# Kernel tuning notes

Measured on AMD Instinct MI355X. Metric: run time of the kernel, lower is better.

The kernel has to match this reference:

```python
import jax, jax.numpy as jnp
import numpy as np

N = 50000      # nodes
E = 1_600_000  # edges
F_IN = 128; HID = 128; LAT = 64; OUT = 128; GEN = 2


def gcn_conv(x, src, dst, norm, W, b, n_nodes):
    """PyG GCNConv with self-loops already appended to (src, dst) and
    symmetric normalization `norm` precomputed per edge."""
    h = x @ W                                    # [N, out]
    msg = h[src] * norm[:, None]                 # [E+N, out] gather + scale
    out = jax.ops.segment_sum(msg, dst, num_segments=n_nodes)
    return out + b


def _self_loop_norm(edge_index, n_nodes):
    loops = jnp.arange(n_nodes, dtype=edge_index.dtype)
    src = jnp.concatenate([edge_index[0], loops])
    dst = jnp.concatenate([edge_index[1], loops])
    deg = jnp.zeros((n_nodes,), jnp.float32).at[dst].add(1.0)
    dinv = jnp.where(deg > 0, deg ** -0.5, 0.0)
    norm = dinv[src] * dinv[dst]
    return src, dst, norm


def setup_inputs() -> dict:
    key = jax.random.key(0)
    ks = jax.random.split(key, 12)
    p = lambda k, s: jax.random.normal(k, s, jnp.float32) * 0.05
    return {
        "x": jax.random.normal(ks[0], (N, F_IN), jnp.float32),
        "edge_index": jax.random.randint(ks[1], (2, E), 0, N, jnp.int32),
        "eps": jax.random.normal(ks[2], (N, LAT), jnp.float32),
        "u": jax.random.uniform(ks[3], (N, GEN), jnp.float32),
        "W1": p(ks[4], (F_IN, HID)), "b1": jnp.zeros((HID,), jnp.float32),
        "W_mu": p(ks[5], (HID, LAT)), "b_mu": jnp.zeros((LAT,), jnp.float32),
        "W_ls": p(ks[6], (HID, LAT)), "b_ls": jnp.zeros((LAT,), jnp.float32),
        "W_dx": p(ks[7], (LAT, OUT)), "b_dx": jnp.zeros((OUT,), jnp.float32),
        "W_g": p(ks[8], (LAT, GEN)), "b_g": jnp.zeros((GEN,), jnp.float32),
        "W_lc": p(ks[9], (LAT, 1)), "b_lc": jnp.zeros((1,), jnp.float32),
    }


def reference(x, edge_index, eps, u, W1, b1, W_mu, b_mu, W_ls, b_ls,
              W_dx, b_dx, W_g, b_g, W_lc, b_lc):
    n = x.shape[0]
    src, dst, norm = _self_loop_norm(edge_index, n)

    # Encoder: GCN -> relu -> (mu, logvar)
    h = jax.nn.relu(gcn_conv(x, src, dst, norm, W1, b1, n))
    mu = gcn_conv(h, src, dst, norm, W_mu, b_mu, n)
    logvar = gcn_conv(h, src, dst, norm, W_ls, b_ls, n)

    # reparameterize: z = eps * exp(0.5*logvar) + mu
    z = eps * jnp.exp(0.5 * logvar) + mu

    # decoders / classifiers
    recon_x = gcn_conv(z, src, dst, norm, W_dx, b_dx, n)
    logits_gender = gcn_conv(z, src, dst, norm, W_g, b_g, n)
    logits_label = z @ W_lc + b_lc

    # Gumbel-softmax (hard, straight-through), temperature=1.0
    g = -jnp.log(-jnp.log(u + 1e-20) + 1e-20)
    y_soft = jax.nn.softmax(logits_gender + g, axis=-1)
    y_hard = jax.nn.one_hot(jnp.argmax(y_soft, axis=-1), GEN, dtype=y_soft.dtype)
    gender = jax.lax.stop_gradient(y_hard - y_soft) + y_soft

    return (recon_x, gender, logits_label, mu, logvar, z)
```

## Files before the change

kernel.cpp:

```cpp
#include <hip/hip_runtime.h>
#include <hip/hip_fp16.h>
#include <cstddef>


constexpr int R = 200;
constexpr int NBUCK = 250;
constexpr int NBLK = 250;
constexpr int SLABCAP = 12288;

__device__ __forceinline__ void gemm_tile32(
    int tile, const float* __restrict__ A, const float* __restrict__ W,
    __half* __restrict__ Ch, int n, float* sW) {
  constexpr int K = 128, M = 128, KT = 64, RPT = 4, CG = 32;
  const int tid = threadIdx.x;
  const int cgi = tid % CG;
  const int rs = tid / CG;
  const int row0 = tile * 32 + rs * RPT;

  const float* Arow[RPT];
#pragma unroll
  for (int rr = 0; rr < RPT; ++rr) {
    int row = row0 + rr;
    if (row > n - 1) row = n - 1;
    Arow[rr] = A + (size_t)row * K;
  }
  float4 acc[RPT];
#pragma unroll
  for (int rr = 0; rr < RPT; ++rr) acc[rr] = float4{0.f, 0.f, 0.f, 0.f};

  for (int kt = 0; kt < K; kt += KT) {
    if (kt) __syncthreads();
    for (int i = tid * 4; i < KT * M; i += 1024)
      *reinterpret_cast<float4*>(&sW[i]) =
          *reinterpret_cast<const float4*>(&W[kt * M + i]);
    __syncthreads();
#pragma unroll 4
    for (int k4 = 0; k4 < KT; k4 += 4) {
      float4 a[RPT];
#pragma unroll
      for (int rr = 0; rr < RPT; ++rr)
        a[rr] = *reinterpret_cast<const float4*>(Arow[rr] + kt + k4);
#pragma unroll
      for (int j = 0; j < 4; ++j) {
        float4 w2 = *reinterpret_cast<const float4*>(&sW[(k4 + j) * M + cgi * 4]);
#pragma unroll
        for (int rr = 0; rr < RPT; ++rr) {
          float av = reinterpret_cast<const float*>(&a[rr])[j];
          acc[rr].x += av * w2.x; acc[rr].y += av * w2.y;
          acc[rr].z += av * w2.z; acc[rr].w += av * w2.w;
        }
      }
    }
  }
#pragma unroll
  for (int rr = 0; rr < RPT; ++rr) {
    int row = row0 + rr;
    if (row < n) {
      __half2* d2 = reinterpret_cast<__half2*>(Ch + (size_t)row * M + cgi * 4);
      d2[0] = __floats2half2_rn(acc[rr].x, acc[rr].y);
      d2[1] = __floats2half2_rn(acc[rr].z, acc[rr].w);
    }
  }
}

union HistSmem { int h[NBUCK]; float sW[64 * 128]; };
__global__ __launch_bounds__(256, 4) void hist_gemm_kernel(
    const int* __restrict__ dst, int* __restrict__ gh, int e, int chunk,
    const float* __restrict__ A, const float* __restrict__ W,
    __half* __restrict__ Ch, int n, int tbase) {
  __shared__ HistSmem sm;
  if (blockIdx.x < (unsigned)NBLK) {
    for (int t = threadIdx.x; t < NBUCK; t += 256) sm.h[t] = 0;
    __syncthreads();
    int beg = blockIdx.x * chunk;
    int fin = min(e, beg + chunk);
    for (int i = beg + threadIdx.x; i < fin; i += 256)
      atomicAdd(&sm.h[dst[i] / R], 1);
    __syncthreads();
    for (int t = threadIdx.x; t < NBUCK; t += 256)
      gh[t * NBLK + blockIdx.x] = sm.h[t];
  } else {
    gemm_tile32(tbase + (blockIdx.x - NBLK), A, W, Ch, n, sm.sW);
  }
}

union BscanSmem { struct { int s[256]; int sBase[NBUCK + 1]; } b; float sW[64 * 128]; };
__global__ __launch_bounds__(256, 4) void bscan_gemm_kernel(
    const int* __restrict__ gh, int* __restrict__ ghs,
    int* __restrict__ rowptr_n,
    const float* __restrict__ A, const float* __restrict__ W,
    __half* __restrict__ Ch, int n, int tbase) {
  __shared__ BscanSmem sm;
  const int tid = threadIdx.x;
  if (blockIdx.x < (unsigned)NBUCK) {
    const int b = blockIdx.x;
    int tot = 0;
    if (tid < NBUCK) {
      const int* row = gh + tid * NBLK;
      for (int k = 0; k < NBLK; ++k) tot += row[k];
    }
    sm.b.s[tid] = tot;
    __syncthreads();
    for (int off = 1; off < 256; off <<= 1) {
      int t = (tid >= off) ? sm.b.s[tid - off] : 0;
      __syncthreads();
      sm.b.s[tid] += t;
      __syncthreads();
    }
    if (tid < NBUCK) sm.b.sBase[tid] = sm.b.s[tid] - tot;
    if (tid == NBUCK - 1) sm.b.sBase[NBUCK] = sm.b.s[tid];
    __syncthreads();

    int v = (tid < NBLK) ? gh[b * NBLK + tid] : 0;
    sm.b.s[tid] = v;
    __syncthreads();
    for (int off = 1; off < 256; off <<= 1) {
      int t = (tid >= off) ? sm.b.s[tid - off] : 0;
      __syncthreads();
      sm.b.s[tid] += t;
      __syncthreads();
    }
    if (tid < NBLK) ghs[b * NBLK + tid] = sm.b.s[tid] - v + sm.b.sBase[b];
    if (b == 0 && tid == 0) *rowptr_n = sm.b.sBase[NBUCK];
  } else {
    gemm_tile32(tbase + (blockIdx.x - NBUCK), A, W, Ch, n, sm.sW);
  }
}

union ScatSmem { int cur[NBUCK]; float sW[64 * 128]; };
__global__ __launch_bounds__(256, 4) void scatter_gemm_kernel(
    const int* __restrict__ src, const int* __restrict__ dst,
    const int* __restrict__ ghs, int* __restrict__ binned, int e, int chunk,
    const float* __restrict__ A, const float* __restrict__ W,
    __half* __restrict__ Ch, int n, int tbase) {
  __shared__ ScatSmem sm;
  if (blockIdx.x < (unsigned)NBLK) {
    for (int t = threadIdx.x; t < NBUCK; t += 256)
      sm.cur[t] = ghs[t * NBLK + blockIdx.x];
    __syncthreads();
    int beg = blockIdx.x * chunk;
    int fin = min(e, beg + chunk);
    for (int i = beg + threadIdx.x; i < fin; i += 256) {
      int d = dst[i];
      int b = d / R;
      int p = atomicAdd(&sm.cur[b], 1);
      binned[p] = ((d - b * R) << 16) | src[i];
    }
  } else {
    gemm_tile32(tbase + (blockIdx.x - NBLK), A, W, Ch, n, sm.sW);
  }
}

union FinSmem {
  struct { int sdeg[R]; int sscan[256]; int scur[R]; int slab[SLABCAP]; } f;
  float sW[64 * 128];
};
__global__ __launch_bounds__(256, 3) void final_gemm_kernel(
    const int* __restrict__ binned, const int* __restrict__ ghs,
    int* __restrict__ rowptr, int* __restrict__ csr,
    float* __restrict__ dinv, int n, int e,
    const float* __restrict__ A, const float* __restrict__ W,
    __half* __restrict__ Ch, int tbase, int T) {
  __shared__ FinSmem sm;
  const int tid = threadIdx.x;
  if (blockIdx.x < (unsigned)NBUCK) {
    const int b = blockIdx.x;
    const int base = ghs[b * NBLK];
    const int endv = (b < NBUCK - 1) ? ghs[(b + 1) * NBLK] : e;
    const int cnt = endv - base;

    if (tid < R) sm.f.sdeg[tid] = 0;
    __syncthreads();
    for (int k = base + tid; k < endv; k += 256)
      atomicAdd(&sm.f.sdeg[binned[k] >> 16], 1);
    __syncthreads();

    int dv = (tid < R) ? sm.f.sdeg[tid] : 0;
    sm.f.sscan[tid] = dv;
    __syncthreads();
    for (int off = 1; off < 256; off <<= 1) {
      int t = (tid >= off) ? sm.f.sscan[tid - off] : 0;
      __syncthreads();
      sm.f.sscan[tid] += t;
      __syncthreads();
    }
    int excl = sm.f.sscan[tid] - dv;
    int node = b * R + tid;
    if (tid < R && node < n) {
      rowptr[node] = base + excl;
      dinv[node] = 1.0f / sqrtf((float)dv + 1.0f);
      sm.f.scur[tid] = excl;
    }
    __syncthreads();

    const bool fits = (cnt <= SLABCAP);
    for (int k = base + tid; k < endv; k += 256) {
      int rec = binned[k];
      int p = atomicAdd(&sm.f.scur[rec >> 16], 1);
      int s = rec & 0xFFFF;
      if (fits) sm.f.slab[p] = s;
      else csr[base + p] = s;
    }
    __syncthreads();
    if (fits)
      for (int k = tid; k < cnt; k += 256) csr[base + k] = sm.f.slab[k];
  } else {
    int t0 = tbase + (blockIdx.x - NBUCK);
    if (t0 < T) gemm_tile32(t0, A, W, Ch, n, sm.sW);
  }
}

template <int K, int M, int KT, int RPT, bool BIAS>
__global__ __launch_bounds__(256, 4) void gemm_kernel(
    const float* __restrict__ A, const float* __restrict__ W,
    const float* __restrict__ bias, float* __restrict__ C, int n) {
  constexpr int CG = M / 4;
  constexpr int RS = 256 / CG;
  constexpr int RPB = RS * RPT;
  __shared__ float sW[KT * M];
  const int cg = threadIdx.x % CG;
  const int rs = threadIdx.x / CG;
  const int row0 = blockIdx.x * RPB + rs * RPT;

  const float* Arow[RPT];
#pragma unroll
  for (int rr = 0; rr < RPT; ++rr) {
    int row = row0 + rr;
    if (row > n - 1) row = n - 1;
    Arow[rr] = A + (size_t)row * K;
  }

  float4 acc[RPT];
#pragma unroll
  for (int rr = 0; rr < RPT; ++rr) acc[rr] = float4{0.f, 0.f, 0.f, 0.f};

  for (int kt = 0; kt < K; kt += KT) {
    if (kt) __syncthreads();
    for (int i = threadIdx.x * 4; i < KT * M; i += 1024)
      *reinterpret_cast<float4*>(&sW[i]) =
          *reinterpret_cast<const float4*>(&W[kt * M + i]);
    __syncthreads();
#pragma unroll 4
    for (int k4 = 0; k4 < KT; k4 += 4) {
      float4 a[RPT];
#pragma unroll
      for (int rr = 0; rr < RPT; ++rr)
        a[rr] = *reinterpret_cast<const float4*>(Arow[rr] + kt + k4);
#pragma unroll
      for (int j = 0; j < 4; ++j) {
        float4 w = *reinterpret_cast<const float4*>(&sW[(k4 + j) * M + cg * 4]);
#pragma unroll
        for (int rr = 0; rr < RPT; ++rr) {
          float av = reinterpret_cast<const float*>(&a[rr])[j];
          acc[rr].x += av * w.x;
          acc[rr].y += av * w.y;
          acc[rr].z += av * w.z;
          acc[rr].w += av * w.w;
        }
      }
    }
  }

  float4 bv = float4{0.f, 0.f, 0.f, 0.f};
  if (BIAS) bv = *reinterpret_cast<const float4*>(&bias[cg * 4]);
#pragma unroll
  for (int rr = 0; rr < RPT; ++rr) {
    int row = row0 + rr;
    if (row < n) {
      float4 o = acc[rr];
      if (BIAS) { o.x += bv.x; o.y += bv.y; o.z += bv.z; o.w += bv.w; }
      *reinterpret_cast<float4*>(&C[(size_t)row * M + cg * 4]) = o;
    }
  }
}

template <bool SRCSCALE, bool BIAS, bool RELU, bool HALF_OUT>
__global__ __launch_bounds__(256) void spmm128_kernel(
    const __half* __restrict__ Xs, void* __restrict__ Yout,
    const int* __restrict__ rowptr, const int* __restrict__ csr,
    const float* __restrict__ dinv, const float* __restrict__ bias, int n) {
  int wid = (blockIdx.x * blockDim.x + threadIdx.x) >> 6;
  int lane = threadIdx.x & 63;
  if (wid >= n) return;
  int beg = rowptr[wid];
  int end = rowptr[wid + 1];
  constexpr int U = 8;
  float a0[U], a1[U];
#pragma unroll
  for (int uu = 0; uu < U; ++uu) { a0[uu] = 0.f; a1[uu] = 0.f; }

  for (int base = beg; base < end; base += 64) {
    int m = end - base;
    if (m > 64) m = 64;
    int idx = (lane < m) ? csr[base + lane] : 0;
    int j = 0;
    for (; j + U <= m; j += U) {
      const __half2* rows[U];
      float ds[U];
#pragma unroll
      for (int uu = 0; uu < U; ++uu) {
        int i = __shfl(idx, j + uu, 64);
        rows[uu] = reinterpret_cast<const __half2*>(Xs + (size_t)i * 128);
        if (SRCSCALE) ds[uu] = dinv[i];
      }
      __half2 v[U];
#pragma unroll
      for (int uu = 0; uu < U; ++uu) v[uu] = rows[uu][lane];
#pragma unroll
      for (int uu = 0; uu < U; ++uu) {
        float2 f = __half22float2(v[uu]);
        if (SRCSCALE) {
          a0[uu] += ds[uu] * f.x;
          a1[uu] += ds[uu] * f.y;
        } else {
          a0[uu] += f.x;
          a1[uu] += f.y;
        }
      }
    }
    for (; j < m; ++j) {
      int i = __shfl(idx, j, 64);
      const __half2* row = reinterpret_cast<const __half2*>(Xs + (size_t)i * 128);
      float2 f = __half22float2(row[lane]);
      if (SRCSCALE) {
        float ds = dinv[i];
        a0[0] += ds * f.x;
        a1[0] += ds * f.y;
      } else {
        a0[0] += f.x;
        a1[0] += f.y;
      }
    }
  }

  float t0 = 0.f, t1 = 0.f;
#pragma unroll
  for (int uu = 0; uu < U; ++uu) { t0 += a0[uu]; t1 += a1[uu]; }

  float di = dinv[wid];

  float2 sf = __half22float2(
      reinterpret_cast<const __half2*>(Xs + (size_t)wid * 128)[lane]);
  if (SRCSCALE) {
    t0 += di * sf.x;
    t1 += di * sf.y;
  } else {
    t0 += sf.x;
    t1 += sf.y;
  }

  float r0 = di * t0;
  float r1 = di * t1;
  if (BIAS) { r0 += bias[lane * 2]; r1 += bias[lane * 2 + 1]; }
  if (RELU) { r0 = fmaxf(r0, 0.f); r1 = fmaxf(r1, 0.f); }

  if (HALF_OUT) {
    reinterpret_cast<__half2*>((__half*)Yout + (size_t)wid * 128)[lane] =
        __floats2half2_rn(di * r0, di * r1);
  } else {
    float2 o = {r0, r1};
    reinterpret_cast<float2*>((float*)Yout + (size_t)wid * 128)[lane] = o;
  }
}

__global__ __launch_bounds__(256, 4) void mlz_kernel(
    const float* __restrict__ hagg,
    const float* __restrict__ Wmu, const float* __restrict__ bmu,
    const float* __restrict__ Wls, const float* __restrict__ bls,
    const float* __restrict__ eps, const float* __restrict__ dinv,
    const float* __restrict__ Wg, const float* __restrict__ Wlc,
    const float* __restrict__ blc,
    float* __restrict__ out_mu, float* __restrict__ out_lv,
    float* __restrict__ out_z, unsigned int* __restrict__ zh8,
    float2* __restrict__ zgs, float* __restrict__ out_label, int n) {
  constexpr int K = 128, M = 64, KT = 64, RPT = 4;
  constexpr int CG = M / 4;
  constexpr int RS = 256 / CG;
  constexpr int RPB = RS * RPT;
  __shared__ float sWm[KT * M];
  __shared__ float sWl[KT * M];
  const int cg = threadIdx.x % CG;
  const int rs = threadIdx.x / CG;
  const int row0 = blockIdx.x * RPB + rs * RPT;

  const float* Arow[RPT];
#pragma unroll
  for (int rr = 0; rr < RPT; ++rr) {
    int row = row0 + rr;
    if (row > n - 1) row = n - 1;
    Arow[rr] = hagg + (size_t)row * K;
  }

  float4 am[RPT], al[RPT];
#pragma unroll
  for (int rr = 0; rr < RPT; ++rr) {
    am[rr] = float4{0.f, 0.f, 0.f, 0.f};
    al[rr] = float4{0.f, 0.f, 0.f, 0.f};
  }

  for (int kt = 0; kt < K; kt += KT) {
    if (kt) __syncthreads();
    for (int i = threadIdx.x * 4; i < KT * M; i += 1024) {
      *reinterpret_cast<float4*>(&sWm[i]) =
          *reinterpret_cast<const float4*>(&Wmu[kt * M + i]);
      *reinterpret_cast<float4*>(&sWl[i]) =
          *reinterpret_cast<const float4*>(&Wls[kt * M + i]);
    }
    __syncthreads();
#pragma unroll 2
    for (int k4 = 0; k4 < KT; k4 += 4) {
      float4 a[RPT];
#pragma unroll
      for (int rr = 0; rr < RPT; ++rr)
        a[rr] = *reinterpret_cast<const float4*>(Arow[rr] + kt + k4);
#pragma unroll
      for (int j = 0; j < 4; ++j) {
        float4 wm = *reinterpret_cast<const float4*>(&sWm[(k4 + j) * M + cg * 4]);
        float4 wl = *reinterpret_cast<const float4*>(&sWl[(k4 + j) * M + cg * 4]);
#pragma unroll
        for (int rr = 0; rr < RPT; ++rr) {
          float av = reinterpret_cast<const float*>(&a[rr])[j];
          am[rr].x += av * wm.x; am[rr].y += av * wm.y;
          am[rr].z += av * wm.z; am[rr].w += av * wm.w;
          al[rr].x += av * wl.x; al[rr].y += av * wl.y;
          al[rr].z += av * wl.z; al[rr].w += av * wl.w;
        }
      }
    }
  }

  float4 bm = *reinterpret_cast<const float4*>(&bmu[cg * 4]);
  float4 bl = *reinterpret_cast<const float4*>(&bls[cg * 4]);
  float wg0[4], wg1[4], wlcv[4];
#pragma unroll
  for (int cc = 0; cc < 4; ++cc) {
    int c = cg * 4 + cc;
    wg0[cc] = Wg[c * 2 + 0];
    wg1[cc] = Wg[c * 2 + 1];
    wlcv[cc] = Wlc[c];
  }
  float blc0 = blc[0];

#pragma unroll
  for (int rr = 0; rr < RPT; ++rr) {
    int row = row0 + rr;
    if (row < n) {
      float4 mu4 = {am[rr].x + bm.x, am[rr].y + bm.y,
                    am[rr].z + bm.z, am[rr].w + bm.w};
      float4 lv4 = {al[rr].x + bl.x, al[rr].y + bl.y,
                    al[rr].z + bl.z, al[rr].w + bl.w};
      float4 e4 = *reinterpret_cast<const float4*>(&eps[(size_t)row * 64 + cg * 4]);
      float4 z4 = {e4.x * expf(0.5f * lv4.x) + mu4.x,
                   e4.y * expf(0.5f * lv4.y) + mu4.y,
                   e4.z * expf(0.5f * lv4.z) + mu4.z,
                   e4.w * expf(0.5f * lv4.w) + mu4.w};
      *reinterpret_cast<float4*>(&out_mu[(size_t)row * 64 + cg * 4]) = mu4;
      *reinterpret_cast<float4*>(&out_lv[(size_t)row * 64 + cg * 4]) = lv4;
      *reinterpret_cast<float4*>(&out_z[(size_t)row * 64 + cg * 4]) = z4;
      float di = dinv[row];
      int pw = __builtin_amdgcn_cvt_pk_fp8_f32(di * z4.x, di * z4.y, 0, false);
      pw = __builtin_amdgcn_cvt_pk_fp8_f32(di * z4.z, di * z4.w, pw, true);
      zh8[(size_t)row * 16 + cg] = (unsigned int)pw;
      float pg0 = z4.x * wg0[0] + z4.y * wg0[1] + z4.z * wg0[2] + z4.w * wg0[3];
      float pg1 = z4.x * wg1[0] + z4.y * wg1[1] + z4.z * wg1[2] + z4.w * wg1[3];
      float pl  = z4.x * wlcv[0] + z4.y * wlcv[1] + z4.z * wlcv[2] + z4.w * wlcv[3];
#pragma unroll
      for (int off = 1; off < 16; off <<= 1) {
        pg0 += __shfl_xor(pg0, off, 64);
        pg1 += __shfl_xor(pg1, off, 64);
        pl  += __shfl_xor(pl, off, 64);
      }
      if (cg == 0) {
        zgs[row] = float2{di * pg0, di * pg1};
        out_label[row] = pl + blc0;
      }
    }
  }
}

__device__ __forceinline__ void fp8x4acc(unsigned d, float* a) {
#if defined(__has_builtin) && __has_builtin(__builtin_amdgcn_cvt_pk_f32_fp8)
  typedef float f32x2 __attribute__((ext_vector_type(2)));
  f32x2 lo = __builtin_amdgcn_cvt_pk_f32_fp8((int)d, false);
  f32x2 hi = __builtin_amdgcn_cvt_pk_f32_fp8((int)d, true);
  a[0] += lo.x; a[1] += lo.y; a[2] += hi.x; a[3] += hi.y;
#else
  a[0] += __builtin_amdgcn_cvt_f32_fp8((int)d, 0);
  a[1] += __builtin_amdgcn_cvt_f32_fp8((int)d, 1);
  a[2] += __builtin_amdgcn_cvt_f32_fp8((int)d, 2);
  a[3] += __builtin_amdgcn_cvt_f32_fp8((int)d, 3);
#endif
}

__global__ __launch_bounds__(256) void spmm_zg_kernel(
    const unsigned char* __restrict__ zh8, const float2* __restrict__ zgs,
    float* __restrict__ zagg, const int* __restrict__ rowptr,
    const int* __restrict__ csr, const float* __restrict__ dinv,
    const float* __restrict__ bg, const float* __restrict__ u,
    float* __restrict__ out_gender, int n) {
  int wid = (blockIdx.x * blockDim.x + threadIdx.x) >> 6;
  int lane = threadIdx.x & 63;
  if (wid >= n) return;
  int beg = rowptr[wid];
  int end = rowptr[wid + 1];
  const int g = lane >> 4;
  const int c = lane & 15;
  const int coff = c * 4;

  float accA[4], accB[4];
#pragma unroll
  for (int f = 0; f < 4; ++f) { accA[f] = 0.f; accB[f] = 0.f; }
  float ga0 = 0.f, ga1 = 0.f;

  for (int base = beg; base < end; base += 64) {
    int m = end - base;
    if (m > 64) m = 64;
    int idx = 0;
    if (lane < m) {
      idx = csr[base + lane];
      float2 gz = zgs[idx];
      ga0 += gz.x;
      ga1 += gz.y;
    }
    int j = 0;
    for (; j + 8 <= m; j += 8) {
      int i0 = __shfl(idx, j + g, 64);
      int i1 = __shfl(idx, j + 4 + g, 64);
      unsigned d0 = *reinterpret_cast<const unsigned*>(
          zh8 + (size_t)(unsigned)i0 * 64 + coff);
      unsigned d1 = *reinterpret_cast<const unsigned*>(
          zh8 + (size_t)(unsigned)i1 * 64 + coff);
      fp8x4acc(d0, accA);
      fp8x4acc(d1, accB);
    }
    if (j < m) {
      int e0 = j + g;
      int e1 = j + 4 + g;
      int i0 = __shfl(idx, min(e0, m - 1), 64);
      int i1 = __shfl(idx, min(e1, m - 1), 64);
      unsigned d0 = *reinterpret_cast<const unsigned*>(
          zh8 + (size_t)(unsigned)i0 * 64 + coff);
      unsigned d1 = *reinterpret_cast<const unsigned*>(
          zh8 + (size_t)(unsigned)i1 * 64 + coff);
      if (e0 >= m) d0 = 0u;
      if (e1 >= m) d1 = 0u;
      fp8x4acc(d0, accA);
      fp8x4acc(d1, accB);
    }
  }

  float t[4];
#pragma unroll
  for (int f = 0; f < 4; ++f) t[f] = accA[f] + accB[f];
#pragma unroll
  for (int f = 0; f < 4; ++f) t[f] += __shfl_xor(t[f], 16, 64);
#pragma unroll
  for (int f = 0; f < 4; ++f) t[f] += __shfl_xor(t[f], 32, 64);

  float di = dinv[wid];
  if (lane < 16) {
    unsigned ds = *reinterpret_cast<const unsigned*>(
        zh8 + (size_t)wid * 64 + coff);
    fp8x4acc(ds, t);
    float4 o = {di * t[0], di * t[1], di * t[2], di * t[3]};
    *reinterpret_cast<float4*>(&zagg[(size_t)wid * 64 + 4 * c]) = o;
  }

  for (int off = 32; off > 0; off >>= 1) {
    ga0 += __shfl_xor(ga0, off, 64);
    ga1 += __shfl_xor(ga1, off, 64);
  }
  if (lane == 0) {
    float2 self = zgs[wid];
    ga0 += self.x;
    ga1 += self.y;
    float lg0 = di * ga0 + bg[0];
    float lg1 = di * ga1 + bg[1];
    float u0 = u[(size_t)wid * 2 + 0];
    float u1 = u[(size_t)wid * 2 + 1];
    float g0 = -logf(-logf(u0 + 1e-20f) + 1e-20f);
    float g1 = -logf(-logf(u1 + 1e-20f) + 1e-20f);
    float a0 = lg0 + g0, a1 = lg1 + g1;
    float mx = fmaxf(a0, a1);
    float e0 = expf(a0 - mx), e1 = expf(a1 - mx);
    float s = e0 + e1;
    float y0 = e0 / s, y1 = e1 / s;
    float h0 = (y1 > y0) ? 0.f : 1.f;
    float h1 = 1.f - h0;
    out_gender[(size_t)wid * 2 + 0] = (h0 - y0) + y0;
    out_gender[(size_t)wid * 2 + 1] = (h1 - y1) + y1;
  }
}

extern "C" void kernel_launch(void* const* d_in, const int* in_sizes, int n_in,
                              void* d_out, int out_size, void* d_ws, size_t ws_size,
                              hipStream_t stream) {
  const float* x   = (const float*)d_in[0];
  const int*   ei  = (const int*)d_in[1];
  const float* eps = (const float*)d_in[2];
  const float* u   = (const float*)d_in[3];
  const float* W1  = (const float*)d_in[4];
  const float* b1  = (const float*)d_in[5];
  const float* Wmu = (const float*)d_in[6];
  const float* bmu = (const float*)d_in[7];
  const float* Wls = (const float*)d_in[8];
  const float* bls = (const float*)d_in[9];
  const float* Wdx = (const float*)d_in[10];
  const float* bdx = (const float*)d_in[11];
  const float* Wg  = (const float*)d_in[12];
  const float* bg  = (const float*)d_in[13];
  const float* Wlc = (const float*)d_in[14];
  const float* blc = (const float*)d_in[15];

  const int n = in_sizes[0] / 128;
  const int e = in_sizes[1] / 2;
  const int* esrc = ei;
  const int* edst = ei + e;

  float* out = (float*)d_out;
  float* out_recon  = out;
  float* out_gender = out + (size_t)n * 128;
  float* out_label  = out_gender + (size_t)n * 2;
  float* out_mu     = out_label + n;
  float* out_lv     = out_mu + (size_t)n * 64;
  float* out_z      = out_lv + (size_t)n * 64;

  char* w = (char*)d_ws;
  size_t off = 0;
  auto alloc = [&](size_t bytes) {
    char* p = w + off;
    off = (off + bytes + 255) & ~(size_t)255;
    return p;
  };
  float* dinv  = (float*)alloc((size_t)n * 4);
  int* rowptr  = (int*)alloc((size_t)(n + 1) * 4);
  int* csr     = (int*)alloc((size_t)e * 4);
  int* gh      = (int*)alloc((size_t)NBUCK * NBLK * 4);
  int* ghs     = (int*)alloc((size_t)NBUCK * NBLK * 4);
  __half* Xs   = (__half*)alloc((size_t)n * 128 * 2);
  __half* hb   = (__half*)alloc((size_t)n * 128 * 2);
  float2* zgs  = (float2*)alloc((size_t)n * 8);
  unsigned char* zh8 = (unsigned char*)Xs;
  float* zagg  = (float*)hb;
  float* hagg  = out_recon;
  int* binned  = (int*)out_lv;

  const int chunk = (e + NBLK - 1) / NBLK;
  const int GBLK = (n + 31) / 32;
  const int T = GBLK;

  const int TH = 500, TB = 450, TS = 350;
  const int TF = T - TH - TB - TS;

  hist_gemm_kernel<<<NBLK + TH, 256, 0, stream>>>(
      edst, gh, e, chunk, x, W1, Xs, n, 0);
  bscan_gemm_kernel<<<NBUCK + TB, 256, 0, stream>>>(
      gh, ghs, &rowptr[n], x, W1, Xs, n, TH);
  scatter_gemm_kernel<<<NBLK + TS, 256, 0, stream>>>(
      esrc, edst, ghs, binned, e, chunk, x, W1, Xs, n, TH + TB);
  final_gemm_kernel<<<NBUCK + TF, 256, 0, stream>>>(
      binned, ghs, rowptr, csr, dinv, n, e, x, W1, Xs, TH + TB + TS, T);

  spmm128_kernel<true, true, true, true>
      <<<(n + 3) / 4, 256, 0, stream>>>(Xs, hb, rowptr, csr, dinv, b1, n);
  spmm128_kernel<false, false, false, false>
      <<<(n + 3) / 4, 256, 0, stream>>>(hb, hagg, rowptr, csr, dinv, nullptr, n);
  mlz_kernel<<<(n + 63) / 64, 256, 0, stream>>>(
      hagg, Wmu, bmu, Wls, bls, eps, dinv, Wg, Wlc, blc,
      out_mu, out_lv, out_z, (unsigned int*)zh8, zgs, out_label, n);
  spmm_zg_kernel<<<(n + 3) / 4, 256, 0, stream>>>(
      zh8, (const float2*)zgs, zagg, rowptr, csr, dinv, bg, u, out_gender, n);
  gemm_kernel<64, 128, 64, 4, true>
      <<<GBLK, 256, 0, stream>>>(zagg, Wdx, bdx, out_recon, n);
}
```

Before: 397.4 us.

## Replace per-chunk bucket scan with global atomic cursors in CSR build

The CSR construction drops the 250-block per-(bucket,chunk) offset scan. It now uses a single-block scan over bucket totals plus global atomic cursors that each chunk claims during scatter, which means scatter re-histograms its chunk. Buckets shrink to 100 nodes (500 buckets) with 512 chunks, a smaller slab, and higher occupancy for the final kernel. The GEMM tile split across the four fused kernels is rebalanced. Edge order within a bucket becomes nondeterministic, and scatter does an extra pass over dst.

```diff
diff --git a/kernel.cpp b/kernel.cpp
--- a/kernel.cpp
+++ b/kernel.cpp
@@ -3,10 +3,10 @@
 #include <cstddef>
 
 
-constexpr int R = 200;
-constexpr int NBUCK = 250;
-constexpr int NBLK = 250;
-constexpr int SLABCAP = 12288;
+constexpr int RB = 100;
+constexpr int NBUCK = 500;
+constexpr int NCH = 512;
+constexpr int SLABCAP = 6400;
 
 __device__ __forceinline__ void gemm_tile32(
     int tile, const float* __restrict__ A, const float* __restrict__ W,
@@ -65,98 +65,100 @@
 
 union HistSmem { int h[NBUCK]; float sW[64 * 128]; };
 __global__ __launch_bounds__(256, 4) void hist_gemm_kernel(
-    const int* __restrict__ dst, int* __restrict__ gh, int e, int chunk,
+    const int* __restrict__ dst, int* __restrict__ gcnt, int e, int chunk,
     const float* __restrict__ A, const float* __restrict__ W,
     __half* __restrict__ Ch, int n, int tbase) {
   __shared__ HistSmem sm;
-  if (blockIdx.x < (unsigned)NBLK) {
+  if (blockIdx.x < (unsigned)NCH) {
     for (int t = threadIdx.x; t < NBUCK; t += 256) sm.h[t] = 0;
     __syncthreads();
     int beg = blockIdx.x * chunk;
     int fin = min(e, beg + chunk);
     for (int i = beg + threadIdx.x; i < fin; i += 256)
-      atomicAdd(&sm.h[dst[i] / R], 1);
+      atomicAdd(&sm.h[dst[i] / RB], 1);
     __syncthreads();
     for (int t = threadIdx.x; t < NBUCK; t += 256)
-      gh[t * NBLK + blockIdx.x] = sm.h[t];
+      gcnt[blockIdx.x * NBUCK + t] = sm.h[t];
   } else {
-    gemm_tile32(tbase + (blockIdx.x - NBLK), A, W, Ch, n, sm.sW);
-  }
-}
-
-union BscanSmem { struct { int s[256]; int sBase[NBUCK + 1]; } b; float sW[64 * 128]; };
-__global__ __launch_bounds__(256, 4) void bscan_gemm_kernel(
-    const int* __restrict__ gh, int* __restrict__ ghs,
-    int* __restrict__ rowptr_n,
+    gemm_tile32(tbase + (blockIdx.x - NCH), A, W, Ch, n, sm.sW);
+  }
+}
+
+union ScanSmem { struct { int s[512]; int tot[NBUCK]; } b; float sW[64 * 128]; };
+__global__ __launch_bounds__(256, 4) void scan_gemm_kernel(
+    const int* __restrict__ gcnt, int* __restrict__ bbase,
+    int* __restrict__ gcur, int* __restrict__ rowptr_n, int e,
     const float* __restrict__ A, const float* __restrict__ W,
     __half* __restrict__ Ch, int n, int tbase) {
-  __shared__ BscanSmem sm;
+  __shared__ ScanSmem sm;
   const int tid = threadIdx.x;
-  if (blockIdx.x < (unsigned)NBUCK) {
-    const int b = blockIdx.x;
-    int tot = 0;
-    if (tid < NBUCK) {
-      const int* row = gh + tid * NBLK;
-      for (int k = 0; k < NBLK; ++k) tot += row[k];
-    }
-    sm.b.s[tid] = tot;
-    __syncthreads();
-    for (int off = 1; off < 256; off <<= 1) {
-      int t = (tid >= off) ? sm.b.s[tid - off] : 0;
+  if (blockIdx.x == 0) {
+    for (int b = tid; b < 512; b += 256) {
+      int tot = 0;
+      if (b < NBUCK)
+        for (int c = 0; c < NCH; ++c) tot += gcnt[c * NBUCK + b];
+      sm.b.s[b] = tot;
+      if (b < NBUCK) sm.b.tot[b] = tot;
+    }
+    __syncthreads();
+    for (int off = 1; off < 512; off <<= 1) {
+      int i0 = tid, i1 = tid + 256;
+      int v0 = (i0 >= off) ? sm.b.s[i0 - off] : 0;
+      int v1 = (i1 >= off) ? sm.b.s[i1 - off] : 0;
       __syncthreads();
-      sm.b.s[tid] += t;
+      sm.b.s[i0] += v0;
+      sm.b.s[i1] += v1;
       __syncthreads();
     }
-    if (tid < NBUCK) sm.b.sBase[tid] = sm.b.s[tid] - tot;
-    if (tid == NBUCK - 1) sm.b.sBase[NBUCK] = sm.b.s[tid];
-    __syncthreads();
-
-    int v = (tid < NBLK) ? gh[b * NBLK + tid] : 0;
-    sm.b.s[tid] = v;
-    __syncthreads();
-    for (int off = 1; off < 256; off <<= 1) {
-      int t = (tid >= off) ? sm.b.s[tid - off] : 0;
-      __syncthreads();
-      sm.b.s[tid] += t;
-      __syncthreads();
-    }
-    if (tid < NBLK) ghs[b * NBLK + tid] = sm.b.s[tid] - v + sm.b.sBase[b];
-    if (b == 0 && tid == 0) *rowptr_n = sm.b.sBase[NBUCK];
+    for (int b = tid; b < NBUCK; b += 256) {
+      int ex = sm.b.s[b] - sm.b.tot[b];
+      bbase[b] = ex;
+      gcur[b] = ex;
+    }
+    if (tid == 0) { bbase[NBUCK] = e; *rowptr_n = e; }
   } else {
-    gemm_tile32(tbase + (blockIdx.x - NBUCK), A, W, Ch, n, sm.sW);
-  }
-}
-
-union ScatSmem { int cur[NBUCK]; float sW[64 * 128]; };
+    gemm_tile32(tbase + (blockIdx.x - 1), A, W, Ch, n, sm.sW);
+  }
+}
+
+union ScatSmem { int h[NBUCK]; float sW[64 * 128]; };
 __global__ __launch_bounds__(256, 4) void scatter_gemm_kernel(
     const int* __restrict__ src, const int* __restrict__ dst,
-    const int* __restrict__ ghs, int* __restrict__ binned, int e, int chunk,
+    int* __restrict__ gcur, int* __restrict__ binned, int e, int chunk,
     const float* __restrict__ A, const float* __restrict__ W,
     __half* __restrict__ Ch, int n, int tbase) {
   __shared__ ScatSmem sm;
-  if (blockIdx.x < (unsigned)NBLK) {
-    for (int t = threadIdx.x; t < NBUCK; t += 256)
-      sm.cur[t] = ghs[t * NBLK + blockIdx.x];
+  if (blockIdx.x < (unsigned)NCH) {
+    for (int t = threadIdx.x; t < NBUCK; t += 256) sm.h[t] = 0;
     __syncthreads();
     int beg = blockIdx.x * chunk;
     int fin = min(e, beg + chunk);
+    for (int i = beg + threadIdx.x; i < fin; i += 256)
+      atomicAdd(&sm.h[dst[i] / RB], 1);
+    __syncthreads();
+    for (int t = threadIdx.x; t < NBUCK; t += 256) {
+      int c = sm.h[t];
+      int r = (c > 0) ? atomicAdd(&gcur[t], c) : 0;
+      sm.h[t] = r;
+    }
+    __syncthreads();
     for (int i = beg + threadIdx.x; i < fin; i += 256) {
       int d = dst[i];
-      int b = d / R;
-      int p = atomicAdd(&sm.cur[b], 1);
-      binned[p] = ((d - b * R) << 16) | src[i];
+      int b = d / RB;
+      int p = atomicAdd(&sm.h[b], 1);
+      binned[p] = ((d - b * RB) << 16) | src[i];
     }
   } else {
-    gemm_tile32(tbase + (blockIdx.x - NBLK), A, W, Ch, n, sm.sW);
+    gemm_tile32(tbase + (blockIdx.x - NCH), A, W, Ch, n, sm.sW);
   }
 }
 
 union FinSmem {
-  struct { int sdeg[R]; int sscan[256]; int scur[R]; int slab[SLABCAP]; } f;
+  struct { int sdeg[RB]; int sscan[256]; int scur[RB]; int slab[SLABCAP]; } f;
   float sW[64 * 128];
 };
-__global__ __launch_bounds__(256, 3) void final_gemm_kernel(
-    const int* __restrict__ binned, const int* __restrict__ ghs,
+__global__ __launch_bounds__(256, 4) void final_gemm_kernel(
+    const int* __restrict__ binned, const int* __restrict__ bbase,
     int* __restrict__ rowptr, int* __restrict__ csr,
     float* __restrict__ dinv, int n, int e,
     const float* __restrict__ A, const float* __restrict__ W,
@@ -165,17 +167,17 @@
   const int tid = threadIdx.x;
   if (blockIdx.x < (unsigned)NBUCK) {
     const int b = blockIdx.x;
-    const int base = ghs[b * NBLK];
-    const int endv = (b < NBUCK - 1) ? ghs[(b + 1) * NBLK] : e;
+    const int base = bbase[b];
+    const int endv = bbase[b + 1];
     const int cnt = endv - base;
 
-    if (tid < R) sm.f.sdeg[tid] = 0;
+    if (tid < RB) sm.f.sdeg[tid] = 0;
     __syncthreads();
     for (int k = base + tid; k < endv; k += 256)
       atomicAdd(&sm.f.sdeg[binned[k] >> 16], 1);
     __syncthreads();
 
-    int dv = (tid < R) ? sm.f.sdeg[tid] : 0;
+    int dv = (tid < RB) ? sm.f.sdeg[tid] : 0;
     sm.f.sscan[tid] = dv;
     __syncthreads();
     for (int off = 1; off < 256; off <<= 1) {
@@ -185,8 +187,8 @@
       __syncthreads();
     }
     int excl = sm.f.sscan[tid] - dv;
-    int node = b * R + tid;
-    if (tid < R && node < n) {
+    int node = b * RB + tid;
+    if (tid < RB && node < n) {
       rowptr[node] = base + excl;
       dinv[node] = 1.0f / sqrtf((float)dv + 1.0f);
       sm.f.scur[tid] = excl;
@@ -635,8 +637,9 @@
   float* dinv  = (float*)alloc((size_t)n * 4);
   int* rowptr  = (int*)alloc((size_t)(n + 1) * 4);
   int* csr     = (int*)alloc((size_t)e * 4);
-  int* gh      = (int*)alloc((size_t)NBUCK * NBLK * 4);
-  int* ghs     = (int*)alloc((size_t)NBUCK * NBLK * 4);
+  int* gcnt    = (int*)alloc((size_t)NCH * NBUCK * 4);
+  int* bbase   = (int*)alloc((size_t)(NBUCK + 1) * 4);
+  int* gcur    = (int*)alloc((size_t)NBUCK * 4);
   __half* Xs   = (__half*)alloc((size_t)n * 128 * 2);
   __half* hb   = (__half*)alloc((size_t)n * 128 * 2);
   float2* zgs  = (float2*)alloc((size_t)n * 8);
@@ -645,21 +648,21 @@
   float* hagg  = out_recon;
   int* binned  = (int*)out_lv;
 
-  const int chunk = (e + NBLK - 1) / NBLK;
+  const int chunk = (e + NCH - 1) / NCH;
   const int GBLK = (n + 31) / 32;
   const int T = GBLK;
 
-  const int TH = 500, TB = 450, TS = 350;
-  const int TF = T - TH - TB - TS;
-
-  hist_gemm_kernel<<<NBLK + TH, 256, 0, stream>>>(
-      edst, gh, e, chunk, x, W1, Xs, n, 0);
-  bscan_gemm_kernel<<<NBUCK + TB, 256, 0, stream>>>(
-      gh, ghs, &rowptr[n], x, W1, Xs, n, TH);
-  scatter_gemm_kernel<<<NBLK + TS, 256, 0, stream>>>(
-      esrc, edst, ghs, binned, e, chunk, x, W1, Xs, n, TH + TB);
-  final_gemm_kernel<<<NBUCK + TF, 256, 0, stream>>>(
-      binned, ghs, rowptr, csr, dinv, n, e, x, W1, Xs, TH + TB + TS, T);
+  const int T1 = 420, T2 = 460, T3 = 420;
+  const int T4 = T - T1 - T2 - T3;
+
+  hist_gemm_kernel<<<NCH + T1, 256, 0, stream>>>(
+      edst, gcnt, e, chunk, x, W1, Xs, n, 0);
+  scan_gemm_kernel<<<1 + T2, 256, 0, stream>>>(
+      gcnt, bbase, gcur, &rowptr[n], e, x, W1, Xs, n, T1);
+  scatter_gemm_kernel<<<NCH + T3, 256, 0, stream>>>(
+      esrc, edst, gcur, binned, e, chunk, x, W1, Xs, n, T1 + T2);
+  final_gemm_kernel<<<NBUCK + T4, 256, 0, stream>>>(
+      binned, bbase, rowptr, csr, dinv, n, e, x, W1, Xs, T1 + T2 + T3, T);
 
   spmm128_kernel<true, true, true, true>
       <<<(n + 3) / 4, 256, 0, stream>>>(Xs, hb, rowptr, csr, dinv, b1, n);
```

Measured after the change: 415.1 us. +4.4%, slower.
